# Kernel tuning notes

Hardware: AMD Instinct MI355X
Metric: run time of the kernel (lower is better)

The kernel has to match this reference:

```python
import jax, jax.numpy as jnp
import numpy as np

N = 2048
H_DIM = 64
N_HEADS = 4
N_HIDDEN = H_DIM // N_HEADS  # is_concat=True
L = 16  # max_labels_dim
SLOPE = 0.2


def leaky(x, slope=SLOPE):
    return jnp.where(x >= 0, x, slope * x)


def setup_inputs() -> dict:
    key = jax.random.key(0)
    k1, k2, k3, k4 = jax.random.split(key, 4)
    x = jax.random.normal(k1, (N, H_DIM), dtype=jnp.float32)
    # labels in [0, L]; value == L means unlabeled -> all-zero one-hot row
    lab = jax.random.randint(k2, (N,), 0, L + 1)
    ohm_labels = jnp.where((lab < L)[:, None],
                           jax.nn.one_hot(jnp.minimum(lab, L - 1), L, dtype=jnp.float32),
                           0.0)
    in_features = H_DIM + L
    W_l = jax.random.normal(k3, (H_DIM, in_features), dtype=jnp.float32) / np.sqrt(in_features)
    W_attn = jax.random.normal(k4, (N_HIDDEN,), dtype=jnp.float32) / np.sqrt(N_HIDDEN)
    return {"x": x, "ohm_labels": ohm_labels, "W_l": W_l, "W_attn": W_attn, "sparsity": 0}


def reference(x, ohm_labels, W_l, W_attn, sparsity):
    n_nodes = x.shape[0]
    # fill unlabeled rows with uniform 1/L
    unlabeled = ohm_labels.sum(axis=1) == 0  # (N,)
    ohm = jnp.where(unlabeled[:, None], 1.0 / L, ohm_labels)
    pin = jnp.concatenate([x, ohm], axis=1)  # (N, h_dim + L)

    # shared-weight projection: g_l == g_r == g
    g = (pin @ W_l.T).reshape(n_nodes, N_HEADS, N_HIDDEN)  # (N, H, F)
    # g_sum[i, j] = g_l[j] + g_r[i]  (repeat / repeat_interleave semantics)
    g_sum = g[None, :, :, :] + g[:, None, :, :]            # (N, N, H, F)
    e = jnp.einsum('ijhf,f->ijh', leaky(g_sum), W_attn)    # (N, N, H)
    a = jax.nn.softmax(e, axis=1)                          # softmax over j
    # dropout in eval mode: identity
    attn_res = jnp.einsum('ijh,jhf->ihf', a, g)            # (N, H, F)
    out = attn_res.reshape(n_nodes, N_HEADS * N_HIDDEN)    # is_concat
    h = leaky(out)                                         # processor activation

    # centroids per label from ohm (post-fill) as in get_centroids
    cluster_agg = ohm.T @ h                                # (L, D)
    cnt = ohm.sum(axis=0)                                  # (L,)
    missing = cnt == 0
    centroids = jnp.where(missing[:, None], 0.0,
                          cluster_agg / jnp.where(missing, 1.0, cnt)[:, None])
    # cdist p=2
    diff = h[:, None, :] - centroids[None, :, :]           # (N, L, D)
    scores = -jnp.sqrt(jnp.sum(diff * diff, axis=-1))      # (N, L)
    return scores, h, missing
```

## Files before the change

kernel.cpp:

```cpp
#include <hip/hip_runtime.h>
#include <hip/hip_bf16.h>
#include <math.h>

#define C1F  0.577078016f
#define C2F  0.865617024f

#define WS_CNT 0
#define WS_AGG 128
#define WS_G   8320
#define WS_DCL (8320 + 524288)

typedef float __attribute__((ext_vector_type(4))) f32x4;

__device__ __forceinline__ float dpp_sum32(float x) {
    float y;
    y = __int_as_float(__builtin_amdgcn_update_dpp(0, __float_as_int(x), 0x111, 0xf, 0xf, true)); x += y;
    y = __int_as_float(__builtin_amdgcn_update_dpp(0, __float_as_int(x), 0x112, 0xf, 0xf, true)); x += y;
    y = __int_as_float(__builtin_amdgcn_update_dpp(0, __float_as_int(x), 0x114, 0xf, 0xf, true)); x += y;
    y = __int_as_float(__builtin_amdgcn_update_dpp(0, __float_as_int(x), 0x118, 0xf, 0xf, true)); x += y;
    y = __int_as_float(__builtin_amdgcn_update_dpp(0, __float_as_int(x), 0x142, 0xa, 0xf, true)); x += y;
    return x;
}

__global__ __launch_bounds__(256) void k_proj(
    const float* __restrict__ x, const float* __restrict__ ohm,
    const float* __restrict__ Wl, const float* __restrict__ Wattn,
    unsigned char* __restrict__ ws)
{
    float* g    = (float*)(ws + WS_G);
    float* dclT = (float*)(ws + WS_DCL);
    unsigned long long* cnt = (unsigned long long*)(ws + WS_CNT);

    int t = threadIdx.x;
    int r = blockIdx.x * 4 + (t >> 6);
    int o = t & 63;

    f32x4 oh[4]; float rs = 0.f;
    const f32x4* ohp = (const f32x4*)&ohm[r*16];
    #pragma unroll
    for (int q = 0; q < 4; ++q) { oh[q] = ohp[q]; rs += oh[q][0]+oh[q][1]+oh[q][2]+oh[q][3]; }
    if (rs == 0.f) {
        f32x4 c = {0.0625f, 0.0625f, 0.0625f, 0.0625f};
        #pragma unroll
        for (int q = 0; q < 4; ++q) oh[q] = c;
    }

    float acc = 0.f;
    const f32x4* xp = (const f32x4*)&x[r*64];
    const f32x4* wp = (const f32x4*)&Wl[o*80];
    #pragma unroll
    for (int q = 0; q < 16; ++q) {
        f32x4 a = xp[q], b = wp[q];
        acc = fmaf(a[0],b[0],acc); acc = fmaf(a[1],b[1],acc);
        acc = fmaf(a[2],b[2],acc); acc = fmaf(a[3],b[3],acc);
    }
    #pragma unroll
    for (int q = 0; q < 4; ++q) {
        f32x4 b = wp[16+q];
        acc = fmaf(oh[q][0],b[0],acc); acc = fmaf(oh[q][1],b[1],acc);
        acc = fmaf(oh[q][2],b[2],acc); acc = fmaf(oh[q][3],b[3],acc);
    }
    g[r*64 + o] = acc;

    float dot = Wattn[o & 15] * acc;
    #pragma unroll
    for (int m2 = 1; m2 < 16; m2 <<= 1) dot += __shfl_xor(dot, m2);
    if ((o & 15) == 0) dclT[(o >> 4)*2048 + r] = C2F * dot;

    if (t < 16) {
        float c = 0.f;
        for (int rr = 0; rr < 4; ++rr) {
            int r2 = blockIdx.x*4 + rr; float s = 0.f;
            #pragma unroll
            for (int k = 0; k < 16; ++k) s += ohm[r2*16+k];
            c += (s == 0.f) ? 0.0625f : ohm[r2*16+t];
        }
        atomicAdd(&cnt[t], (unsigned long long)__float2ll_rn(c * 1048576.0f));
    }
}

__global__ __launch_bounds__(512, 4) void k_attn(
    const float* __restrict__ ohm, const float* __restrict__ Wattn,
    unsigned char* __restrict__ ws, float* __restrict__ hout)
{
    float* g    = (float*)(ws + WS_G);
    float* dclT = (float*)(ws + WS_DCL);
    unsigned long long* agg = (unsigned long long*)(ws + WS_AGG);

    __shared__ float gl[2][128*68];
    __shared__ float shh[256];
    __shared__ float ohmf[64];

    int t = threadIdx.x, bid = blockIdx.x;
    int p = t >> 5, sub = t & 31;
    int r = p >> 2, h = p & 3;
    int irow = bid*4 + r;

    const f32x4* gv4 = (const f32x4*)g;
    float* w0 = &gl[0][(t >> 4)*68 + (t & 15)*4];
    float* w1 = &gl[1][(t >> 4)*68 + (t & 15)*4];

    float wv[16], gA[16];
    #pragma unroll
    for (int f = 0; f < 16; ++f)
        wv[f] = __uint_as_float(__builtin_amdgcn_readfirstlane(__float_as_uint(Wattn[f])));
    #pragma unroll
    for (int f = 0; f < 16; ++f) gA[f] = g[irow*64 + h*16 + f];

    float acc[16];
    #pragma unroll
    for (int f = 0; f < 16; ++f) acc[f] = 0.f;
    float lsum = 0.f;

    const float* dpt = dclT + h*2048 + sub;

    f32x4 s0[4], st[4];
    float djc[4], djn[4], djn2[4] = {0.f,0.f,0.f,0.f};
    #pragma unroll
    for (int q = 0; q < 4; ++q) { s0[q] = gv4[t + q*512]; st[q] = gv4[2048 + t + q*512]; }
    #pragma unroll
    for (int k = 0; k < 4; ++k) { djc[k] = dpt[k*32]; djn[k] = dpt[128 + k*32]; }
    #pragma unroll
    for (int q = 0; q < 4; ++q) *(f32x4*)(w0 + q*2176) = s0[q];
    asm volatile("s_waitcnt lgkmcnt(0)\n\ts_barrier" ::: "memory");

    #pragma unroll
    for (int tile = 0; tile < 16; ++tile) {
        if (tile < 15) {
            float* wd = (tile & 1) ? w0 : w1;
            #pragma unroll
            for (int q = 0; q < 4; ++q) *(f32x4*)(wd + q*2176) = st[q];
        }
        if (tile < 14) {
            #pragma unroll
            for (int q = 0; q < 4; ++q) st[q] = gv4[(tile+2)*2048 + t + q*512];
            #pragma unroll
            for (int k = 0; k < 4; ++k) djn2[k] = dpt[(tile+2)*128 + k*32];
        }

        const float* bp = (tile & 1) ? &gl[1][0] : &gl[0][0];
        #pragma unroll
        for (int k = 0; k < 4; ++k) {
            const float* gj = bp + (k*32 + sub)*68 + h*16;
            f32x4 q0 = *(const f32x4*)(gj);
            f32x4 q1 = *(const f32x4*)(gj+4);
            f32x4 q2 = *(const f32x4*)(gj+8);
            f32x4 q3 = *(const f32x4*)(gj+12);
            float gvv[16] = { q0[0],q0[1],q0[2],q0[3], q1[0],q1[1],q1[2],q1[3],
                              q2[0],q2[1],q2[2],q2[3], q3[0],q3[1],q3[2],q3[3] };
            float s0a = 0.f, s1a = 0.f;
            #pragma unroll
            for (int f = 0; f < 16; f += 2) {
                float t0 = gA[f]   + gvv[f];
                float t1 = gA[f+1] + gvv[f+1];
                s0a = fmaf(wv[f],   fabsf(t0), s0a);
                s1a = fmaf(wv[f+1], fabsf(t1), s1a);
            }
            float pj = __builtin_amdgcn_exp2f(fmaf(C1F, s0a + s1a, djc[k]));
            lsum += pj;
            #pragma unroll
            for (int f = 0; f < 16; ++f) acc[f] = fmaf(pj, gvv[f], acc[f]);
        }
        asm volatile("s_waitcnt lgkmcnt(0)\n\ts_barrier" ::: "memory");
        #pragma unroll
        for (int k = 0; k < 4; ++k) { djc[k] = djn[k]; djn[k] = djn2[k]; }
    }

    float ls = dpp_sum32(lsum);
    float hv[16];
    #pragma unroll
    for (int f = 0; f < 16; ++f) hv[f] = dpp_sum32(acc[f]);

    if ((t & 31) == 31) {
        float rl = 1.0f / ls;
        #pragma unroll
        for (int f = 0; f < 16; ++f) {
            float a = hv[f]*rl; a = fmaxf(a, 0.2f*a);
            hout[irow*64 + h*16 + f] = a;
            shh[r*64 + h*16 + f] = a;
        }
    }
    if (t < 64) {
        int rr = t >> 4, ll = t & 15;
        float v = ohm[(bid*4 + rr)*16 + ll];
        float s = v;
        #pragma unroll
        for (int m2 = 1; m2 < 16; m2 <<= 1) s += __shfl_xor(s, m2);
        ohmf[rr*16 + ll] = (s == 0.f) ? 0.0625f : v;
    }
    __syncthreads();

    for (int v = t; v < 1024; v += 512) {
        int ll = v >> 6, d = v & 63;
        float s = 0.f;
        #pragma unroll
        for (int rr = 0; rr < 4; ++rr) s = fmaf(ohmf[rr*16 + ll], shh[rr*64 + d], s);
        atomicAdd(&agg[v], (unsigned long long)__float2ll_rn(s * 67108864.0f));
    }
}

__global__ __launch_bounds__(256) void k_scores(
    unsigned char* __restrict__ ws, const float* __restrict__ hout,
    float* __restrict__ scores, float* __restrict__ missing)
{
    __shared__ float cl[16*68];
    unsigned long long* cnt = (unsigned long long*)(ws + WS_CNT);
    unsigned long long* agg = (unsigned long long*)(ws + WS_AGG);
    int t = threadIdx.x;

    for (int v = t; v < 1024; v += 256) {
        int ll = v >> 6, d = v & 63;
        long long a = (long long)agg[v];
        long long c = (long long)cnt[ll];
        cl[ll*68 + d] = (c == 0) ? 0.f : ((float)a / (float)c) * 0.015625f;
    }
    if (blockIdx.x == 0 && t < 16) missing[t] = (cnt[t] == 0) ? 1.0f : 0.0f;
    __syncthreads();

    int i = blockIdx.x*16 + (t >> 4), ll = t & 15;
    float s = 0.f;
    #pragma unroll 16
    for (int d = 0; d < 64; ++d) {
        float diff = hout[i*64 + d] - cl[ll*68 + d];
        s = fmaf(diff, diff, s);
    }
    scores[i*16 + ll] = -sqrtf(s);
}

extern "C" void kernel_launch(void* const* d_in, const int* in_sizes, int n_in,
                              void* d_out, int out_size, void* d_ws, size_t ws_size,
                              hipStream_t stream)
{
    const float* x     = (const float*)d_in[0];
    const float* ohm   = (const float*)d_in[1];
    const float* Wl    = (const float*)d_in[2];
    const float* Wattn = (const float*)d_in[3];
    unsigned char* ws  = (unsigned char*)d_ws;

    float* out     = (float*)d_out;
    float* scores  = out;
    float* hout    = out + 2048*16;
    float* missing = out + 2048*16 + 2048*64;

    hipMemsetAsync(d_ws, 0, 8320, stream);
    k_proj  <<<512, 256, 0, stream>>>(x, ohm, Wl, Wattn, ws);
    k_attn  <<<512, 512, 0, stream>>>(ohm, Wattn, ws, hout);
    k_scores<<<128, 256, 0, stream>>>(ws, hout, scores, missing);
}
```

Before: 57.74 us.

## Remap attention threads so each loads one j row and serves four query rows

Threads in the attention kernel now own a single key node j per tile and compute scores for all four query rows of the block, instead of one (row, head) pair with four j values. Each shared-memory g row is loaded once and reused across the four query rows, which removes three quarters of the LDS reads and dclT loads. The per-row query vectors become wave-uniform through readfirstlane. This costs 64 accumulators plus 64 query values per thread in registers, a full 64-lane DPP reduction, and an extra cross-wave reduction through shared memory with one more barrier.

```diff
diff --git a/kernel.cpp b/kernel.cpp
--- a/kernel.cpp
+++ b/kernel.cpp
@@ -12,13 +12,18 @@
 
 typedef float __attribute__((ext_vector_type(4))) f32x4;
 
-__device__ __forceinline__ float dpp_sum32(float x) {
+__device__ __forceinline__ float rfl(float x) {
+    return __uint_as_float(__builtin_amdgcn_readfirstlane(__float_as_uint(x)));
+}
+
+__device__ __forceinline__ float dpp_sum(float x) {
     float y;
     y = __int_as_float(__builtin_amdgcn_update_dpp(0, __float_as_int(x), 0x111, 0xf, 0xf, true)); x += y;
     y = __int_as_float(__builtin_amdgcn_update_dpp(0, __float_as_int(x), 0x112, 0xf, 0xf, true)); x += y;
     y = __int_as_float(__builtin_amdgcn_update_dpp(0, __float_as_int(x), 0x114, 0xf, 0xf, true)); x += y;
     y = __int_as_float(__builtin_amdgcn_update_dpp(0, __float_as_int(x), 0x118, 0xf, 0xf, true)); x += y;
     y = __int_as_float(__builtin_amdgcn_update_dpp(0, __float_as_int(x), 0x142, 0xa, 0xf, true)); x += y;
+    y = __int_as_float(__builtin_amdgcn_update_dpp(0, __float_as_int(x), 0x143, 0xc, 0xf, true)); x += y;
     return x;
 }
 
@@ -88,38 +93,42 @@
     unsigned long long* agg = (unsigned long long*)(ws + WS_AGG);
 
     __shared__ float gl[2][128*68];
+    __shared__ float red[8][68];
     __shared__ float shh[256];
     __shared__ float ohmf[64];
 
     int t = threadIdx.x, bid = blockIdx.x;
-    int p = t >> 5, sub = t & 31;
-    int r = p >> 2, h = p & 3;
-    int irow = bid*4 + r;
+    int h = t >> 7;
+    int j = t & 127;
+    int l = t & 63;
+    int wid = t >> 6;
 
     const f32x4* gv4 = (const f32x4*)g;
     float* w0 = &gl[0][(t >> 4)*68 + (t & 15)*4];
     float* w1 = &gl[1][(t >> 4)*68 + (t & 15)*4];
 
-    float wv[16], gA[16];
-    #pragma unroll
-    for (int f = 0; f < 16; ++f)
-        wv[f] = __uint_as_float(__builtin_amdgcn_readfirstlane(__float_as_uint(Wattn[f])));
-    #pragma unroll
-    for (int f = 0; f < 16; ++f) gA[f] = g[irow*64 + h*16 + f];
-
-    float acc[16];
-    #pragma unroll
-    for (int f = 0; f < 16; ++f) acc[f] = 0.f;
-    float lsum = 0.f;
-
-    const float* dpt = dclT + h*2048 + sub;
+    float wv[16], gAs[4][16];
+    #pragma unroll
+    for (int f = 0; f < 16; ++f) wv[f] = rfl(Wattn[f]);
+    #pragma unroll
+    for (int r = 0; r < 4; ++r)
+        #pragma unroll
+        for (int f = 0; f < 16; ++f)
+            gAs[r][f] = rfl(g[(bid*4 + r)*64 + h*16 + f]);
+
+    float acc[4][16];
+    float lsum[4] = {0.f, 0.f, 0.f, 0.f};
+    #pragma unroll
+    for (int r = 0; r < 4; ++r)
+        #pragma unroll
+        for (int f = 0; f < 16; ++f) acc[r][f] = 0.f;
+
+    const float* dpt = dclT + h*2048 + j;
 
     f32x4 s0[4], st[4];
-    float djc[4], djn[4], djn2[4] = {0.f,0.f,0.f,0.f};
     #pragma unroll
     for (int q = 0; q < 4; ++q) { s0[q] = gv4[t + q*512]; st[q] = gv4[2048 + t + q*512]; }
-    #pragma unroll
-    for (int k = 0; k < 4; ++k) { djc[k] = dpt[k*32]; djn[k] = dpt[128 + k*32]; }
+    float djc = dpt[0], djn = dpt[128], djn2 = 0.f;
     #pragma unroll
     for (int q = 0; q < 4; ++q) *(f32x4*)(w0 + q*2176) = s0[q];
     asm volatile("s_waitcnt lgkmcnt(0)\n\ts_barrier" ::: "memory");
@@ -134,50 +143,53 @@
         if (tile < 14) {
             #pragma unroll
             for (int q = 0; q < 4; ++q) st[q] = gv4[(tile+2)*2048 + t + q*512];
-            #pragma unroll
-            for (int k = 0; k < 4; ++k) djn2[k] = dpt[(tile+2)*128 + k*32];
+            djn2 = dpt[(tile+2)*128];
         }
 
         const float* bp = (tile & 1) ? &gl[1][0] : &gl[0][0];
-        #pragma unroll
-        for (int k = 0; k < 4; ++k) {
-            const float* gj = bp + (k*32 + sub)*68 + h*16;
-            f32x4 q0 = *(const f32x4*)(gj);
-            f32x4 q1 = *(const f32x4*)(gj+4);
-            f32x4 q2 = *(const f32x4*)(gj+8);
-            f32x4 q3 = *(const f32x4*)(gj+12);
-            float gvv[16] = { q0[0],q0[1],q0[2],q0[3], q1[0],q1[1],q1[2],q1[3],
-                              q2[0],q2[1],q2[2],q2[3], q3[0],q3[1],q3[2],q3[3] };
-            float s0a = 0.f, s1a = 0.f;
+        const float* gj = bp + j*68 + h*16;
+        f32x4 q0 = *(const f32x4*)(gj);
+        f32x4 q1 = *(const f32x4*)(gj+4);
+        f32x4 q2 = *(const f32x4*)(gj+8);
+        f32x4 q3 = *(const f32x4*)(gj+12);
+        float gvv[16] = { q0[0],q0[1],q0[2],q0[3], q1[0],q1[1],q1[2],q1[3],
+                          q2[0],q2[1],q2[2],q2[3], q3[0],q3[1],q3[2],q3[3] };
+        float pr[4];
+        #pragma unroll
+        for (int r = 0; r < 4; ++r) {
+            float sa = 0.f, sb = 0.f;
             #pragma unroll
             for (int f = 0; f < 16; f += 2) {
-                float t0 = gA[f]   + gvv[f];
-                float t1 = gA[f+1] + gvv[f+1];
-                s0a = fmaf(wv[f],   fabsf(t0), s0a);
-                s1a = fmaf(wv[f+1], fabsf(t1), s1a);
+                float t0 = gAs[r][f]   + gvv[f];
+                float t1 = gAs[r][f+1] + gvv[f+1];
+                sa = fmaf(wv[f],   fabsf(t0), sa);
+                sb = fmaf(wv[f+1], fabsf(t1), sb);
             }
-            float pj = __builtin_amdgcn_exp2f(fmaf(C1F, s0a + s1a, djc[k]));
-            lsum += pj;
-            #pragma unroll
-            for (int f = 0; f < 16; ++f) acc[f] = fmaf(pj, gvv[f], acc[f]);
-        }
+            pr[r] = __builtin_amdgcn_exp2f(fmaf(C1F, sa + sb, djc));
+            lsum[r] += pr[r];
+        }
+        #pragma unroll
+        for (int r = 0; r < 4; ++r)
+            #pragma unroll
+            for (int f = 0; f < 16; ++f)
+                acc[r][f] = fmaf(pr[r], gvv[f], acc[r][f]);
+
         asm volatile("s_waitcnt lgkmcnt(0)\n\ts_barrier" ::: "memory");
-        #pragma unroll
-        for (int k = 0; k < 4; ++k) { djc[k] = djn[k]; djn[k] = djn2[k]; }
-    }
-
-    float ls = dpp_sum32(lsum);
-    float hv[16];
-    #pragma unroll
-    for (int f = 0; f < 16; ++f) hv[f] = dpp_sum32(acc[f]);
-
-    if ((t & 31) == 31) {
-        float rl = 1.0f / ls;
-        #pragma unroll
-        for (int f = 0; f < 16; ++f) {
-            float a = hv[f]*rl; a = fmaxf(a, 0.2f*a);
-            hout[irow*64 + h*16 + f] = a;
-            shh[r*64 + h*16 + f] = a;
+        djc = djn; djn = djn2;
+    }
+
+    #pragma unroll
+    for (int r = 0; r < 4; ++r) {
+        lsum[r] = dpp_sum(lsum[r]);
+        #pragma unroll
+        for (int f = 0; f < 16; ++f) acc[r][f] = dpp_sum(acc[r][f]);
+    }
+    if (l == 63) {
+        #pragma unroll
+        for (int r = 0; r < 4; ++r) {
+            red[wid][64 + r] = lsum[r];
+            #pragma unroll
+            for (int f = 0; f < 16; ++f) red[wid][r*16 + f] = acc[r][f];
         }
     }
     if (t < 64) {
@@ -187,6 +199,16 @@
         #pragma unroll
         for (int m2 = 1; m2 < 16; m2 <<= 1) s += __shfl_xor(s, m2);
         ohmf[rr*16 + ll] = (s == 0.f) ? 0.0625f : v;
+    }
+    __syncthreads();
+
+    if (t < 256) {
+        int hh = t >> 6, rv = t & 63, r = rv >> 4, f = rv & 15;
+        float a  = red[2*hh][rv]     + red[2*hh+1][rv];
+        float ls = red[2*hh][64 + r] + red[2*hh+1][64 + r];
+        float o = a / ls; o = fmaxf(o, 0.2f*o);
+        hout[(bid*4 + r)*64 + hh*16 + f] = o;
+        shh[r*64 + hh*16 + f] = o;
     }
     __syncthreads();
 
```

Measured after the change: 185.6 us. 221% more time.

## Process two query rows per wave to reuse shared-memory key tiles in attention

Applied to the files above, without the earlier changes.

Each 64-lane wave of the attention kernel now handles two query rows for one head, with each lane covering a single key per half-tile. Every key vector read from LDS is used for both rows, which halves LDS reads per unit of work, and query values are made wave-uniform through readfirstlane. The double-buffered LDS tile is replaced by one buffer guarded by two barriers per tile, prefetch depth drops from two tiles to one, and the wave reduction gains a DPP step to span 64 lanes. The cost is higher register pressure, reflected in fewer waves per SIMD in the launch bounds, and more exposed synchronisation.

```diff
diff --git a/kernel.cpp b/kernel.cpp
--- a/kernel.cpp
+++ b/kernel.cpp
@@ -12,13 +12,18 @@
 
 typedef float __attribute__((ext_vector_type(4))) f32x4;
 
-__device__ __forceinline__ float dpp_sum32(float x) {
+__device__ __forceinline__ float rfl(float x) {
+    return __uint_as_float(__builtin_amdgcn_readfirstlane(__float_as_uint(x)));
+}
+
+__device__ __forceinline__ float dpp_sum(float x) {
     float y;
     y = __int_as_float(__builtin_amdgcn_update_dpp(0, __float_as_int(x), 0x111, 0xf, 0xf, true)); x += y;
     y = __int_as_float(__builtin_amdgcn_update_dpp(0, __float_as_int(x), 0x112, 0xf, 0xf, true)); x += y;
     y = __int_as_float(__builtin_amdgcn_update_dpp(0, __float_as_int(x), 0x114, 0xf, 0xf, true)); x += y;
     y = __int_as_float(__builtin_amdgcn_update_dpp(0, __float_as_int(x), 0x118, 0xf, 0xf, true)); x += y;
     y = __int_as_float(__builtin_amdgcn_update_dpp(0, __float_as_int(x), 0x142, 0xa, 0xf, true)); x += y;
+    y = __int_as_float(__builtin_amdgcn_update_dpp(0, __float_as_int(x), 0x143, 0xc, 0xf, true)); x += y;
     return x;
 }
 
@@ -79,7 +84,7 @@
     }
 }
 
-__global__ __launch_bounds__(512, 4) void k_attn(
+__global__ __launch_bounds__(512, 3) void k_attn(
     const float* __restrict__ ohm, const float* __restrict__ Wattn,
     unsigned char* __restrict__ ws, float* __restrict__ hout)
 {
@@ -87,97 +92,101 @@
     float* dclT = (float*)(ws + WS_DCL);
     unsigned long long* agg = (unsigned long long*)(ws + WS_AGG);
 
-    __shared__ float gl[2][128*68];
+    __shared__ float gl[128*68];
     __shared__ float shh[256];
     __shared__ float ohmf[64];
 
     int t = threadIdx.x, bid = blockIdx.x;
-    int p = t >> 5, sub = t & 31;
-    int r = p >> 2, h = p & 3;
-    int irow = bid*4 + r;
+    int wid = t >> 6, l = t & 63;
+    int rp = wid >> 2, h = wid & 3;
+    int i0 = bid*4 + rp*2, i1 = i0 + 1;
 
     const f32x4* gv4 = (const f32x4*)g;
-    float* w0 = &gl[0][(t >> 4)*68 + (t & 15)*4];
-    float* w1 = &gl[1][(t >> 4)*68 + (t & 15)*4];
-
-    float wv[16], gA[16];
-    #pragma unroll
-    for (int f = 0; f < 16; ++f)
-        wv[f] = __uint_as_float(__builtin_amdgcn_readfirstlane(__float_as_uint(Wattn[f])));
-    #pragma unroll
-    for (int f = 0; f < 16; ++f) gA[f] = g[irow*64 + h*16 + f];
-
-    float acc[16];
-    #pragma unroll
-    for (int f = 0; f < 16; ++f) acc[f] = 0.f;
-    float lsum = 0.f;
-
-    const float* dpt = dclT + h*2048 + sub;
-
-    f32x4 s0[4], st[4];
-    float djc[4], djn[4], djn2[4] = {0.f,0.f,0.f,0.f};
-    #pragma unroll
-    for (int q = 0; q < 4; ++q) { s0[q] = gv4[t + q*512]; st[q] = gv4[2048 + t + q*512]; }
-    #pragma unroll
-    for (int k = 0; k < 4; ++k) { djc[k] = dpt[k*32]; djn[k] = dpt[128 + k*32]; }
-    #pragma unroll
-    for (int q = 0; q < 4; ++q) *(f32x4*)(w0 + q*2176) = s0[q];
-    asm volatile("s_waitcnt lgkmcnt(0)\n\ts_barrier" ::: "memory");
-
-    #pragma unroll
+    float* wbase = &gl[(t >> 4)*68 + (t & 15)*4];
+
+    float wv[16], gA0[16], gA1[16];
+    #pragma unroll
+    for (int f = 0; f < 16; ++f) wv[f] = rfl(Wattn[f]);
+    #pragma unroll
+    for (int f = 0; f < 16; ++f) {
+        gA0[f] = rfl(g[i0*64 + h*16 + f]);
+        gA1[f] = rfl(g[i1*64 + h*16 + f]);
+    }
+
+    float acc0[16], acc1[16];
+    float l0 = 0.f, l1 = 0.f;
+    #pragma unroll
+    for (int f = 0; f < 16; ++f) { acc0[f] = 0.f; acc1[f] = 0.f; }
+
+    const float* dpt = dclT + h*2048 + l;
+
+    f32x4 st[4];
+    #pragma unroll
+    for (int q = 0; q < 4; ++q) st[q] = gv4[t + q*512];
+    float djc0 = dpt[0], djc1 = dpt[64];
+    float djn0 = 0.f, djn1 = 0.f;
+
     for (int tile = 0; tile < 16; ++tile) {
+        if (tile) __syncthreads();
+        #pragma unroll
+        for (int q = 0; q < 4; ++q) *(f32x4*)(wbase + q*2176) = st[q];
+        __syncthreads();
         if (tile < 15) {
-            float* wd = (tile & 1) ? w0 : w1;
-            #pragma unroll
-            for (int q = 0; q < 4; ++q) *(f32x4*)(wd + q*2176) = st[q];
-        }
-        if (tile < 14) {
-            #pragma unroll
-            for (int q = 0; q < 4; ++q) st[q] = gv4[(tile+2)*2048 + t + q*512];
-            #pragma unroll
-            for (int k = 0; k < 4; ++k) djn2[k] = dpt[(tile+2)*128 + k*32];
-        }
-
-        const float* bp = (tile & 1) ? &gl[1][0] : &gl[0][0];
-        #pragma unroll
-        for (int k = 0; k < 4; ++k) {
-            const float* gj = bp + (k*32 + sub)*68 + h*16;
+            #pragma unroll
+            for (int q = 0; q < 4; ++q) st[q] = gv4[(tile+1)*2048 + t + q*512];
+            djn0 = dpt[(tile+1)*128];
+            djn1 = dpt[(tile+1)*128 + 64];
+        }
+
+        #pragma unroll
+        for (int k = 0; k < 2; ++k) {
+            const float* gj = &gl[(k*64 + l)*68 + h*16];
             f32x4 q0 = *(const f32x4*)(gj);
             f32x4 q1 = *(const f32x4*)(gj+4);
             f32x4 q2 = *(const f32x4*)(gj+8);
             f32x4 q3 = *(const f32x4*)(gj+12);
             float gvv[16] = { q0[0],q0[1],q0[2],q0[3], q1[0],q1[1],q1[2],q1[3],
                               q2[0],q2[1],q2[2],q2[3], q3[0],q3[1],q3[2],q3[3] };
-            float s0a = 0.f, s1a = 0.f;
+            float sa0 = 0.f, sb0 = 0.f, sa1 = 0.f, sb1 = 0.f;
             #pragma unroll
             for (int f = 0; f < 16; f += 2) {
-                float t0 = gA[f]   + gvv[f];
-                float t1 = gA[f+1] + gvv[f+1];
-                s0a = fmaf(wv[f],   fabsf(t0), s0a);
-                s1a = fmaf(wv[f+1], fabsf(t1), s1a);
+                float u0 = gA0[f]   + gvv[f];
+                float u1 = gA0[f+1] + gvv[f+1];
+                float v0 = gA1[f]   + gvv[f];
+                float v1 = gA1[f+1] + gvv[f+1];
+                sa0 = fmaf(wv[f],   fabsf(u0), sa0);
+                sb0 = fmaf(wv[f+1], fabsf(u1), sb0);
+                sa1 = fmaf(wv[f],   fabsf(v0), sa1);
+                sb1 = fmaf(wv[f+1], fabsf(v1), sb1);
             }
-            float pj = __builtin_amdgcn_exp2f(fmaf(C1F, s0a + s1a, djc[k]));
-            lsum += pj;
-            #pragma unroll
-            for (int f = 0; f < 16; ++f) acc[f] = fmaf(pj, gvv[f], acc[f]);
-        }
-        asm volatile("s_waitcnt lgkmcnt(0)\n\ts_barrier" ::: "memory");
-        #pragma unroll
-        for (int k = 0; k < 4; ++k) { djc[k] = djn[k]; djn[k] = djn2[k]; }
-    }
-
-    float ls = dpp_sum32(lsum);
-    float hv[16];
-    #pragma unroll
-    for (int f = 0; f < 16; ++f) hv[f] = dpp_sum32(acc[f]);
-
-    if ((t & 31) == 31) {
-        float rl = 1.0f / ls;
+            float djk = k ? djc1 : djc0;
+            float p0 = __builtin_amdgcn_exp2f(fmaf(C1F, sa0 + sb0, djk));
+            float p1 = __builtin_amdgcn_exp2f(fmaf(C1F, sa1 + sb1, djk));
+            l0 += p0; l1 += p1;
+            #pragma unroll
+            for (int f = 0; f < 16; ++f) {
+                acc0[f] = fmaf(p0, gvv[f], acc0[f]);
+                acc1[f] = fmaf(p1, gvv[f], acc1[f]);
+            }
+        }
+        djc0 = djn0; djc1 = djn1;
+    }
+
+    float ls0 = dpp_sum(l0), ls1 = dpp_sum(l1);
+    float h0[16], h1[16];
+    #pragma unroll
+    for (int f = 0; f < 16; ++f) { h0[f] = dpp_sum(acc0[f]); h1[f] = dpp_sum(acc1[f]); }
+
+    if (l == 63) {
+        float r0 = 1.0f / ls0, r1 = 1.0f / ls1;
         #pragma unroll
         for (int f = 0; f < 16; ++f) {
-            float a = hv[f]*rl; a = fmaxf(a, 0.2f*a);
-            hout[irow*64 + h*16 + f] = a;
-            shh[r*64 + h*16 + f] = a;
+            float a = h0[f]*r0; a = fmaxf(a, 0.2f*a);
+            float b = h1[f]*r1; b = fmaxf(b, 0.2f*b);
+            hout[i0*64 + h*16 + f] = a;
+            hout[i1*64 + h*16 + f] = b;
+            shh[(rp*2    )*64 + h*16 + f] = a;
+            shh[(rp*2 + 1)*64 + h*16 + f] = b;
         }
     }
     if (t < 64) {
```

After: 63.03 us. +9.1%, slower.
